# Kernel tuning notes

Hardware: AMD Instinct MI355X
Metric: run time of the kernel (lower is better)

The kernel has to match this reference:

```python
import jax, jax.numpy as jnp
import numpy as np

ALPHA = 0.1          # LeakyReLU negative slope
NEG = -9.0e15        # mask fill value (matches torch source)
S_OUT = 64           # source_out_features
T_OUT = 64           # target_out_features


def setup_inputs() -> dict:
    key = jax.random.key(0)
    ks = jax.random.split(key, 8)
    n_s, n_t = 8192, 4096
    s_in, t_in = 128, 128
    hs = jax.random.normal(ks[0], (n_s, s_in), dtype=jnp.float32)
    ht = jax.random.normal(ks[1], (n_t, t_in), dtype=jnp.float32)
    A_opt = jax.random.randint(ks[2], (n_t, n_s), 0, 2, dtype=jnp.int32)
    # xavier_uniform with gain=1.414
    def xavier(k, shape, gain=1.414):
        fan_in, fan_out = shape[0], shape[1]
        bound = gain * np.sqrt(6.0 / (fan_in + fan_out))
        return jax.random.uniform(k, shape, jnp.float32, -bound, bound)
    Ws = xavier(ks[3], (s_in, T_OUT))
    Wt = xavier(ks[4], (t_in, S_OUT))
    a1 = xavier(ks[5], (S_OUT + T_OUT, 1))
    bias_s = jnp.zeros((T_OUT,), jnp.float32)
    bias_t = jnp.zeros((S_OUT,), jnp.float32)
    return {"hs": hs, "ht": ht, "A_opt": A_opt, "Ws": Ws, "Wt": Wt,
            "a1": a1, "bias_s": bias_s, "bias_t": bias_t}


def reference(hs, ht, A_opt, Ws, Wt, a1, bias_s, bias_t):
    # Asymmetric HOAN, eval mode (dropout=0), concatenate=True.
    Whs = hs @ Ws                       # [n_s, t_out]
    Wht = ht @ Wt                       # [n_t, s_out]
    # a1 split: first S_OUT rows pair with Wht, remaining T_OUT rows with Whs
    a_t = a1[:S_OUT, :]                 # [s_out, 1]
    a_s = a1[S_OUT:, :]                 # [t_out, 1]
    Whst = Whs @ a_s                    # [n_s, 1]
    Whtt = Wht @ a_t                    # [n_t, 1]
    e_st = jax.nn.leaky_relu(Whtt + Whst.T, ALPHA)   # [n_t, n_s]
    e_ts = jax.nn.leaky_relu(Whst + Whtt.T, ALPHA)   # [n_s, n_t]
    mask = A_opt > 0                    # [n_t, n_s]
    att_st = jax.nn.softmax(jnp.where(mask, e_st, NEG), axis=1)
    h_prime_st = att_st @ Whs + bias_s  # [n_t, t_out]
    att_ts = jax.nn.softmax(jnp.where(mask.T, e_ts, NEG), axis=1)
    h_prime_ts = att_ts @ Wht + bias_t  # [n_s, s_out]
    return jax.nn.elu(h_prime_st), jax.nn.elu(h_prime_ts)
```

## Files before the change

### kernel.cpp

```cpp
#include <hip/hip_runtime.h>
#include <math.h>

#define N_S 8192
#define N_T 4096
#define DIN 128
#define NF  64
#define SPL0 8
#define SPL1 8

typedef __attribute__((ext_vector_type(8))) short short8;
typedef __attribute__((ext_vector_type(4))) float f32x4;
typedef unsigned long long u64;
typedef unsigned int u32;

__device__ __forceinline__ unsigned short f2bf(float x){
  unsigned u = __float_as_uint(x);
  unsigned r = (u + 0x7fffu + ((u >> 16) & 1u)) >> 16;
  return (unsigned short)r;
}

__device__ __forceinline__ size_t xt2_idx(int f, int k){
  return ((size_t)(k >> 5))*2048 + (size_t)((f >> 4)*512 + ((k >> 3) & 3)*128 + (f & 15)*8 + (k & 7));
}

__global__ __launch_bounds__(256) void k1_fused(
    const int* __restrict__ A,
    u64* __restrict__ RBt,
    u64* __restrict__ CBt,
    const float* __restrict__ hs, const float* __restrict__ ht,
    const float* __restrict__ Ws, const float* __restrict__ Wt,
    const float* __restrict__ a1,
    unsigned short* __restrict__ XT2s, unsigned short* __restrict__ XT2t,
    float* __restrict__ Es, float* __restrict__ Fs,
    float* __restrict__ Et, float* __restrict__ Ft)
{
  __shared__ __align__(16) float smem[DIN*NF + 4*DIN];
  int bx = blockIdx.x;
  int t = threadIdx.x;
  if (bx < 2048) {
    unsigned* T4 = (unsigned*)smem;
    int i0 = (bx & 63) * 64;
    int j0 = (bx >> 6) * 256;
    int w = t >> 6, l = t & 63;
    int4 v[16];
    #pragma unroll
    for (int it = 0; it < 16; ++it)
      v[it] = *(const int4*)&A[(size_t)(i0 + w*16 + it)*N_S + j0 + 4*l];
    #pragma unroll
    for (int rg = 0; rg < 4; ++rg) {
      unsigned p = 0;
      #pragma unroll
      for (int rr = 0; rr < 4; ++rr) {
        int4 m = v[rg*4 + rr];
        unsigned nib = (m.x > 0 ? 1u : 0u) | (m.y > 0 ? 2u : 0u)
                     | (m.z > 0 ? 4u : 0u) | (m.w > 0 ? 8u : 0u);
        p |= nib << (8*rr);
      }
      T4[(w*4 + rg)*65 + l] = p;
    }
    __syncthreads();
    {
      int r = t & 63, g = t >> 6;
      u64 bits = 0;
      #pragma unroll
      for (int i = 0; i < 16; ++i) {
        unsigned word = T4[(r >> 2)*65 + g*16 + i];
        unsigned nib = (word >> (8*(r & 3))) & 0xFu;
        bits |= (u64)nib << (4*i);
      }
      RBt[(size_t)((j0 >> 6) + g)*N_T + i0 + r] = bits;
    }
    {
      int c = t;
      u64 bits = 0;
      #pragma unroll
      for (int rg = 0; rg < 16; ++rg) {
        unsigned word = T4[rg*65 + (c >> 2)];
        unsigned x = (word >> (c & 3)) & 0x01010101u;
        unsigned nib = (x * 0x01020408u) >> 24;
        bits |= (u64)(nib & 0xFu) << (4*rg);
      }
      CBt[(size_t)(i0 >> 6)*N_S + j0 + c] = bits;
    }
  } else {
    int b = bx - 2048;
    float* Wl = smem;
    float* hrow = smem + DIN*NF;
    bool is_s = b < (N_S/4);
    const float* h; const float* W; const float* av;
    unsigned short* XT; float* Ed; float* Fd; int r0;
    if (is_s) { r0 = b*4;           h = hs; W = Ws; av = a1 + 64; XT = XT2s; Ed = Es; Fd = Fs; }
    else      { r0 = (b - N_S/4)*4; h = ht; W = Wt; av = a1;      XT = XT2t; Ed = Et; Fd = Ft; }
    for (int i = t; i < DIN*NF; i += 256) Wl[i] = W[i];
    for (int i = t; i < 4*DIN;  i += 256) hrow[i] = h[(size_t)r0*DIN + i];
    __syncthreads();
    int f = t & 63, sr = t >> 6;
    float acc = 0.f;
    #pragma unroll 8
    for (int k = 0; k < DIN; ++k) acc += hrow[sr*DIN + k] * Wl[k*NF + f];
    int r = r0 + sr;
    XT[xt2_idx(f, r)] = f2bf(acc);
    float p = acc * av[f];
    #pragma unroll
    for (int o = 32; o > 0; o >>= 1) p += __shfl_xor(p, o, 64);
    if (f == 0) { Ed[r] = __expf(p); Fd[r] = __expf(0.1f*p); }
  }
}

template<int DIR>
__device__ __forceinline__ void agg_body(
    int rb, int split,
    const u64* __restrict__ MBt,
    const float* __restrict__ EuT, const float* __restrict__ FuT,
    const float* __restrict__ EkT, const float* __restrict__ FkT,
    const unsigned short* __restrict__ XT2,
    float* __restrict__ accP,
    float* __restrict__ sumP)
{
  constexpr int NK = (DIR == 0) ? N_S : N_T;
  constexpr int NU = (DIR == 0) ? N_T : N_S;
  constexpr int SPL = (DIR == 0) ? SPL0 : SPL1;
  constexpr int KCH = NK / SPL;
  int t = threadIdx.x;
  int wave = t >> 6, l = t & 63;
  int row16 = l & 15, grp = l >> 4;
  int u = rb*64 + wave*16 + row16;
  float Eu = EuT[u], Fu = FuT[u];
  f32x4 acc[4];
  #pragma unroll
  for (int q = 0; q < 4; ++q) { acc[q][0]=0.f; acc[q][1]=0.f; acc[q][2]=0.f; acc[q][3]=0.f; }
  f32x4 accs; accs[0]=0.f; accs[1]=0.f; accs[2]=0.f; accs[3]=0.f;
  short8 bones;
  #pragma unroll
  for (int j = 0; j < 8; ++j) bones[j] = (short)0x3F80;
  int kc0 = split * KCH;

  #pragma unroll 2
  for (int k0 = kc0; k0 < kc0 + KCH; k0 += 64) {
    u64 mb = MBt[(size_t)(k0 >> 6)*NU + u];
    u32 mlo = (u32)mb, mhi = (u32)(mb >> 32);
    short8 af01[2];
    #pragma unroll
    for (int h = 0; h < 2; ++h) {
      int kb = k0 + 32*h + grp*8;
      float4 e0 = *(const float4*)&EkT[kb];
      float4 e1 = *(const float4*)&EkT[kb + 4];
      float4 f0 = *(const float4*)&FkT[kb];
      float4 f1 = *(const float4*)&FkT[kb + 4];
      float w0 = fmaxf(Eu*e0.x, Fu*f0.x);
      float w1 = fmaxf(Eu*e0.y, Fu*f0.y);
      float w2 = fmaxf(Eu*e0.z, Fu*f0.z);
      float w3 = fmaxf(Eu*e0.w, Fu*f0.w);
      float w4 = fmaxf(Eu*e1.x, Fu*f1.x);
      float w5 = fmaxf(Eu*e1.y, Fu*f1.y);
      float w6 = fmaxf(Eu*e1.z, Fu*f1.z);
      float w7 = fmaxf(Eu*e1.w, Fu*f1.w);
      u32 bb = ((h ? mhi : mlo) >> (grp*8)) & 0xffu;
      float wv[8] = {w0,w1,w2,w3,w4,w5,w6,w7};
      union { u32 uu[4]; short8 v; } pk;
      #pragma unroll
      for (int p = 0; p < 4; ++p) {
        int j = 2*p;
        int slo = ((int)(bb << (31 - j))) >> 31;
        int shi = ((int)(bb << (30 - j))) >> 31;
        u32 msk = __builtin_amdgcn_perm((u32)shi, (u32)slo, 0x05040100u);
        u32 w01 = __builtin_amdgcn_perm(__float_as_uint(wv[j+1]),
                                        __float_as_uint(wv[j]), 0x07060302u);
        pk.uu[p] = w01 & msk;
      }
      af01[h] = pk.v;
    }
    const unsigned short* xb = XT2 + ((size_t)(k0 >> 5))*2048 + l*8;
    #pragma unroll
    for (int q = 0; q < 4; ++q) {
      short8 b0 = *(const short8*)(xb + q*512);
      short8 b1 = *(const short8*)(xb + 2048 + q*512);
      acc[q] = __builtin_amdgcn_mfma_f32_16x16x32_bf16(af01[0], b0, acc[q], 0, 0, 0);
      acc[q] = __builtin_amdgcn_mfma_f32_16x16x32_bf16(af01[1], b1, acc[q], 0, 0, 0);
    }
    accs = __builtin_amdgcn_mfma_f32_16x16x32_bf16(af01[0], bones, accs, 0, 0, 0);
    accs = __builtin_amdgcn_mfma_f32_16x16x32_bf16(af01[1], bones, accs, 0, 0, 0);
  }

  if (row16 == 0) {
    #pragma unroll
    for (int r = 0; r < 4; ++r)
      sumP[(size_t)split*NU + rb*64 + wave*16 + grp*4 + r] = accs[r];
  }
  float* ap = accP + (size_t)split*NU*NF;
  #pragma unroll
  for (int q = 0; q < 4; ++q) {
    #pragma unroll
    for (int r = 0; r < 4; ++r) {
      int uo = rb*64 + wave*16 + grp*4 + r;
      ap[(size_t)uo*NF + q*16 + row16] = acc[q][r];
    }
  }
}

__global__ __launch_bounds__(256, 8) void agg_fused(
    const u64* __restrict__ RBt, const u64* __restrict__ CBt,
    const float* __restrict__ Es, const float* __restrict__ Fs,
    const float* __restrict__ Et, const float* __restrict__ Ft,
    const unsigned short* __restrict__ XT2s, const unsigned short* __restrict__ XT2t,
    float* __restrict__ P0, float* __restrict__ S0,
    float* __restrict__ P1, float* __restrict__ S1)
{
  int b = blockIdx.x;
  if (b < 64*SPL0) {
    agg_body<0>(b & 63, b >> 6, RBt, Et, Ft, Es, Fs, XT2s, P0, S0);
  } else {
    int b2 = b - 64*SPL0;
    agg_body<1>(b2 & 127, b2 >> 7, CBt, Es, Fs, Et, Ft, XT2t, P1, S1);
  }
}

__global__ __launch_bounds__(256) void finalize_kernel(
    const float* __restrict__ P0, const float* __restrict__ S0,
    const float* __restrict__ P1, const float* __restrict__ S1,
    const float* __restrict__ bias_s, const float* __restrict__ bias_t,
    float* __restrict__ out)
{
  int tid = blockIdx.x*256 + threadIdx.x;
  const int n0 = N_T*NF/4;
  float4 a = make_float4(0.f, 0.f, 0.f, 0.f);
  float den = 0.f;
  float4 bias;
  if (tid < n0) {
    int u = tid >> 4, fq = (tid & 15)*4;
    #pragma unroll
    for (int s = 0; s < SPL0; ++s) {
      float4 p = *(const float4*)&P0[((size_t)s*N_T + u)*NF + fq];
      a.x += p.x; a.y += p.y; a.z += p.z; a.w += p.w;
      den += S0[(size_t)s*N_T + u];
    }
    bias = *(const float4*)&bias_s[fq];
  } else {
    int i2 = tid - n0;
    int u = i2 >> 4, fq = (i2 & 15)*4;
    #pragma unroll
    for (int s = 0; s < SPL1; ++s) {
      float4 p = *(const float4*)&P1[((size_t)s*N_S + u)*NF + fq];
      a.x += p.x; a.y += p.y; a.z += p.z; a.w += p.w;
      den += S1[(size_t)s*N_S + u];
    }
    bias = *(const float4*)&bias_t[fq];
  }
  float inv = den > 0.f ? 1.f/den : 0.f;
  float4 v;
  v.x = a.x*inv + bias.x; v.y = a.y*inv + bias.y;
  v.z = a.z*inv + bias.z; v.w = a.w*inv + bias.w;
  v.x = v.x > 0.f ? v.x : expm1f(v.x);
  v.y = v.y > 0.f ? v.y : expm1f(v.y);
  v.z = v.z > 0.f ? v.z : expm1f(v.z);
  v.w = v.w > 0.f ? v.w : expm1f(v.w);
  *(float4*)&out[tid*4] = v;
}

extern "C" void kernel_launch(void* const* d_in, const int* in_sizes, int n_in,
                              void* d_out, int out_size, void* d_ws, size_t ws_size,
                              hipStream_t stream)
{
  const float* hs     = (const float*)d_in[0];
  const float* ht     = (const float*)d_in[1];
  const int*   A      = (const int*)  d_in[2];
  const float* Ws     = (const float*)d_in[3];
  const float* Wt     = (const float*)d_in[4];
  const float* a1     = (const float*)d_in[5];
  const float* bias_s = (const float*)d_in[6];
  const float* bias_t = (const float*)d_in[7];
  float* out = (float*)d_out;

  u64* RBt = (u64*)d_ws;
  u64* CBt = RBt + (size_t)(N_S/64)*N_T;
  unsigned short* XT2s = (unsigned short*)(CBt + (size_t)(N_T/64)*N_S);
  unsigned short* XT2t = XT2s + (size_t)NF*N_S;
  float* Es = (float*)(XT2t + (size_t)NF*N_T);
  float* Fs = Es + N_S;
  float* Et = Fs + N_S;
  float* Ft = Et + N_T;
  float* P0 = Ft + N_T;
  float* S0 = P0 + (size_t)SPL0*N_T*NF;
  float* P1 = S0 + (size_t)SPL0*N_T;
  float* S1 = P1 + (size_t)SPL1*N_S*NF;

  k1_fused<<<2048 + (N_S + N_T)/4, 256, 0, stream>>>(A, RBt, CBt, hs, ht, Ws, Wt, a1,
                                                     XT2s, XT2t, Es, Fs, Et, Ft);
  agg_fused<<<64*SPL0 + 128*SPL1, 256, 0, stream>>>(RBt, CBt, Es, Fs, Et, Ft,
                                                    XT2s, XT2t, P0, S0, P1, S1);
  finalize_kernel<<<(N_T*NF + N_S*NF)/1024, 256, 0, stream>>>(P0, S0, P1, S1,
                                                              bias_s, bias_t, out);
}
```

Before: 89.58 us.

## Fuse finalize into aggregation via last-block counters, interleave E/F, halve split

Removes the separate finalize kernel. Each row block now keeps an atomic counter, and whichever split block finishes last reduces the partial sums, applies bias and ELU, and writes the output. E and F factors are interleaved into one array so a single vector load fetches both, and the target-direction split count drops from 8 to 4, giving fewer partials but also fewer blocks for that direction. This saves one launch and the partial-buffer reread, at the cost of threadfences, an atomic per block, and a serial tail handled by the last block.

```diff
diff --git a/kernel.cpp b/kernel.cpp
--- a/kernel.cpp
+++ b/kernel.cpp
@@ -6,7 +6,7 @@
 #define DIN 128
 #define NF  64
 #define SPL0 8
-#define SPL1 8
+#define SPL1 4
 
 typedef __attribute__((ext_vector_type(8))) short short8;
 typedef __attribute__((ext_vector_type(4))) float f32x4;
@@ -31,12 +31,13 @@
     const float* __restrict__ Ws, const float* __restrict__ Wt,
     const float* __restrict__ a1,
     unsigned short* __restrict__ XT2s, unsigned short* __restrict__ XT2t,
-    float* __restrict__ Es, float* __restrict__ Fs,
-    float* __restrict__ Et, float* __restrict__ Ft)
+    float* __restrict__ EFs, float* __restrict__ EFt,
+    int* __restrict__ cnt)
 {
   __shared__ __align__(16) float smem[DIN*NF + 4*DIN];
   int bx = blockIdx.x;
   int t = threadIdx.x;
+  if (bx == 0 && t < 192) cnt[t] = 0;
   if (bx < 2048) {
     unsigned* T4 = (unsigned*)smem;
     int i0 = (bx & 63) * 64;
@@ -88,9 +89,9 @@
     float* hrow = smem + DIN*NF;
     bool is_s = b < (N_S/4);
     const float* h; const float* W; const float* av;
-    unsigned short* XT; float* Ed; float* Fd; int r0;
-    if (is_s) { r0 = b*4;           h = hs; W = Ws; av = a1 + 64; XT = XT2s; Ed = Es; Fd = Fs; }
-    else      { r0 = (b - N_S/4)*4; h = ht; W = Wt; av = a1;      XT = XT2t; Ed = Et; Fd = Ft; }
+    unsigned short* XT; float* EFd; int r0;
+    if (is_s) { r0 = b*4;           h = hs; W = Ws; av = a1 + 64; XT = XT2s; EFd = EFs; }
+    else      { r0 = (b - N_S/4)*4; h = ht; W = Wt; av = a1;      XT = XT2t; EFd = EFt; }
     for (int i = t; i < DIN*NF; i += 256) Wl[i] = W[i];
     for (int i = t; i < 4*DIN;  i += 256) hrow[i] = h[(size_t)r0*DIN + i];
     __syncthreads();
@@ -103,7 +104,7 @@
     float p = acc * av[f];
     #pragma unroll
     for (int o = 32; o > 0; o >>= 1) p += __shfl_xor(p, o, 64);
-    if (f == 0) { Ed[r] = __expf(p); Fd[r] = __expf(0.1f*p); }
+    if (f == 0) { EFd[2*r] = __expf(p); EFd[2*r + 1] = __expf(0.1f*p); }
   }
 }
 
@@ -111,11 +112,13 @@
 __device__ __forceinline__ void agg_body(
     int rb, int split,
     const u64* __restrict__ MBt,
-    const float* __restrict__ EuT, const float* __restrict__ FuT,
-    const float* __restrict__ EkT, const float* __restrict__ FkT,
+    const float* __restrict__ EFu, const float* __restrict__ EFk,
     const unsigned short* __restrict__ XT2,
     float* __restrict__ accP,
-    float* __restrict__ sumP)
+    float* __restrict__ sumP,
+    int* __restrict__ cnt,
+    const float* __restrict__ bias,
+    float* __restrict__ outB)
 {
   constexpr int NK = (DIR == 0) ? N_S : N_T;
   constexpr int NU = (DIR == 0) ? N_T : N_S;
@@ -125,7 +128,8 @@
   int wave = t >> 6, l = t & 63;
   int row16 = l & 15, grp = l >> 4;
   int u = rb*64 + wave*16 + row16;
-  float Eu = EuT[u], Fu = FuT[u];
+  float2 ef = *(const float2*)&EFu[2*u];
+  float Eu = ef.x, Fu = ef.y;
   f32x4 acc[4];
   #pragma unroll
   for (int q = 0; q < 4; ++q) { acc[q][0]=0.f; acc[q][1]=0.f; acc[q][2]=0.f; acc[q][3]=0.f; }
@@ -143,20 +147,16 @@
     #pragma unroll
     for (int h = 0; h < 2; ++h) {
       int kb = k0 + 32*h + grp*8;
-      float4 e0 = *(const float4*)&EkT[kb];
-      float4 e1 = *(const float4*)&EkT[kb + 4];
-      float4 f0 = *(const float4*)&FkT[kb];
-      float4 f1 = *(const float4*)&FkT[kb + 4];
-      float w0 = fmaxf(Eu*e0.x, Fu*f0.x);
-      float w1 = fmaxf(Eu*e0.y, Fu*f0.y);
-      float w2 = fmaxf(Eu*e0.z, Fu*f0.z);
-      float w3 = fmaxf(Eu*e0.w, Fu*f0.w);
-      float w4 = fmaxf(Eu*e1.x, Fu*f1.x);
-      float w5 = fmaxf(Eu*e1.y, Fu*f1.y);
-      float w6 = fmaxf(Eu*e1.z, Fu*f1.z);
-      float w7 = fmaxf(Eu*e1.w, Fu*f1.w);
+      float4 p0 = *(const float4*)&EFk[2*kb];
+      float4 p1 = *(const float4*)&EFk[2*kb + 4];
+      float4 p2 = *(const float4*)&EFk[2*kb + 8];
+      float4 p3 = *(const float4*)&EFk[2*kb + 12];
+      float wv[8];
+      wv[0] = fmaxf(Eu*p0.x, Fu*p0.y); wv[1] = fmaxf(Eu*p0.z, Fu*p0.w);
+      wv[2] = fmaxf(Eu*p1.x, Fu*p1.y); wv[3] = fmaxf(Eu*p1.z, Fu*p1.w);
+      wv[4] = fmaxf(Eu*p2.x, Fu*p2.y); wv[5] = fmaxf(Eu*p2.z, Fu*p2.w);
+      wv[6] = fmaxf(Eu*p3.x, Fu*p3.y); wv[7] = fmaxf(Eu*p3.z, Fu*p3.w);
       u32 bb = ((h ? mhi : mlo) >> (grp*8)) & 0xffu;
-      float wv[8] = {w0,w1,w2,w3,w4,w5,w6,w7};
       union { u32 uu[4]; short8 v; } pk;
       #pragma unroll
       for (int p = 0; p < 4; ++p) {
@@ -196,65 +196,60 @@
       ap[(size_t)uo*NF + q*16 + row16] = acc[q][r];
     }
   }
-}
-
-__global__ __launch_bounds__(256, 8) void agg_fused(
+
+  __shared__ int sflag;
+  __threadfence();
+  __syncthreads();
+  if (t == 0) sflag = (atomicAdd(cnt, 1) == SPL - 1);
+  __syncthreads();
+  if (!sflag) return;
+  __threadfence();
+  #pragma unroll
+  for (int q = 0; q < 4; ++q) {
+    int item = t + 256*q;
+    int row = item >> 4, f4 = item & 15;
+    int uu = rb*64 + row;
+    float4 a = make_float4(0.f, 0.f, 0.f, 0.f);
+    float den = 0.f;
+    #pragma unroll
+    for (int s = 0; s < SPL; ++s) {
+      float4 p = *(const float4*)&accP[((size_t)s*NU + uu)*NF + f4*4];
+      a.x += p.x; a.y += p.y; a.z += p.z; a.w += p.w;
+      den += sumP[(size_t)s*NU + uu];
+    }
+    float4 b4 = *(const float4*)&bias[f4*4];
+    float inv = den > 0.f ? 1.f/den : 0.f;
+    float4 v;
+    v.x = a.x*inv + b4.x; v.y = a.y*inv + b4.y;
+    v.z = a.z*inv + b4.z; v.w = a.w*inv + b4.w;
+    v.x = v.x > 0.f ? v.x : expm1f(v.x);
+    v.y = v.y > 0.f ? v.y : expm1f(v.y);
+    v.z = v.z > 0.f ? v.z : expm1f(v.z);
+    v.w = v.w > 0.f ? v.w : expm1f(v.w);
+    *(float4*)&outB[(size_t)uu*NF + f4*4] = v;
+  }
+}
+
+__global__ __launch_bounds__(256, 8) void agg_fin(
     const u64* __restrict__ RBt, const u64* __restrict__ CBt,
-    const float* __restrict__ Es, const float* __restrict__ Fs,
-    const float* __restrict__ Et, const float* __restrict__ Ft,
+    const float* __restrict__ EFs, const float* __restrict__ EFt,
     const unsigned short* __restrict__ XT2s, const unsigned short* __restrict__ XT2t,
     float* __restrict__ P0, float* __restrict__ S0,
-    float* __restrict__ P1, float* __restrict__ S1)
+    float* __restrict__ P1, float* __restrict__ S1,
+    int* __restrict__ cnt,
+    const float* __restrict__ bias_s, const float* __restrict__ bias_t,
+    float* __restrict__ out)
 {
   int b = blockIdx.x;
   if (b < 64*SPL0) {
-    agg_body<0>(b & 63, b >> 6, RBt, Et, Ft, Es, Fs, XT2s, P0, S0);
+    int rb = b & 63;
+    agg_body<0>(rb, b >> 6, RBt, EFt, EFs, XT2s, P0, S0, cnt + rb, bias_s, out);
   } else {
     int b2 = b - 64*SPL0;
-    agg_body<1>(b2 & 127, b2 >> 7, CBt, Es, Fs, Et, Ft, XT2t, P1, S1);
-  }
-}
-
-__global__ __launch_bounds__(256) void finalize_kernel(
-    const float* __restrict__ P0, const float* __restrict__ S0,
-    const float* __restrict__ P1, const float* __restrict__ S1,
-    const float* __restrict__ bias_s, const float* __restrict__ bias_t,
-    float* __restrict__ out)
-{
-  int tid = blockIdx.x*256 + threadIdx.x;
-  const int n0 = N_T*NF/4;
-  float4 a = make_float4(0.f, 0.f, 0.f, 0.f);
-  float den = 0.f;
-  float4 bias;
-  if (tid < n0) {
-    int u = tid >> 4, fq = (tid & 15)*4;
-    #pragma unroll
-    for (int s = 0; s < SPL0; ++s) {
-      float4 p = *(const float4*)&P0[((size_t)s*N_T + u)*NF + fq];
-      a.x += p.x; a.y += p.y; a.z += p.z; a.w += p.w;
-      den += S0[(size_t)s*N_T + u];
-    }
-    bias = *(const float4*)&bias_s[fq];
-  } else {
-    int i2 = tid - n0;
-    int u = i2 >> 4, fq = (i2 & 15)*4;
-    #pragma unroll
-    for (int s = 0; s < SPL1; ++s) {
-      float4 p = *(const float4*)&P1[((size_t)s*N_S + u)*NF + fq];
-      a.x += p.x; a.y += p.y; a.z += p.z; a.w += p.w;
-      den += S1[(size_t)s*N_S + u];
-    }
-    bias = *(const float4*)&bias_t[fq];
-  }
-  float inv = den > 0.f ? 1.f/den : 0.f;
-  float4 v;
-  v.x = a.x*inv + bias.x; v.y = a.y*inv + bias.y;
-  v.z = a.z*inv + bias.z; v.w = a.w*inv + bias.w;
-  v.x = v.x > 0.f ? v.x : expm1f(v.x);
-  v.y = v.y > 0.f ? v.y : expm1f(v.y);
-  v.z = v.z > 0.f ? v.z : expm1f(v.z);
-  v.w = v.w > 0.f ? v.w : expm1f(v.w);
-  *(float4*)&out[tid*4] = v;
+    int rb = b2 & 127;
+    agg_body<1>(rb, b2 >> 7, CBt, EFs, EFt, XT2t, P1, S1, cnt + 64 + rb, bias_t,
+                out + (size_t)N_T*NF);
+  }
 }
 
 extern "C" void kernel_launch(void* const* d_in, const int* in_sizes, int n_in,
@@ -275,19 +270,16 @@
   u64* CBt = RBt + (size_t)(N_S/64)*N_T;
   unsigned short* XT2s = (unsigned short*)(CBt + (size_t)(N_T/64)*N_S);
   unsigned short* XT2t = XT2s + (size_t)NF*N_S;
-  float* Es = (float*)(XT2t + (size_t)NF*N_T);
-  float* Fs = Es + N_S;
-  float* Et = Fs + N_S;
-  float* Ft = Et + N_T;
-  float* P0 = Ft + N_T;
-  float* S0 = P0 + (size_t)SPL0*N_T*NF;
-  float* P1 = S0 + (size_t)SPL0*N_T;
-  float* S1 = P1 + (size_t)SPL1*N_S*NF;
+  float* EFs = (float*)(XT2t + (size_t)NF*N_T);
+  float* EFt = EFs + 2*N_S;
+  float* P0  = EFt + 2*N_T;
+  float* S0  = P0 + (size_t)SPL0*N_T*NF;
+  float* P1  = S0 + (size_t)SPL0*N_T;
+  float* S1  = P1 + (size_t)SPL1*N_S*NF;
+  int*   cnt = (int*)(S1 + (size_t)SPL1*N_S);
 
   k1_fused<<<2048 + (N_S + N_T)/4, 256, 0, stream>>>(A, RBt, CBt, hs, ht, Ws, Wt, a1,
-                                                     XT2s, XT2t, Es, Fs, Et, Ft);
-  agg_fused<<<64*SPL0 + 128*SPL1, 256, 0, stream>>>(RBt, CBt, Es, Fs, Et, Ft,
-                                                    XT2s, XT2t, P0, S0, P1, S1);
-  finalize_kernel<<<(N_T*NF + N_S*NF)/1024, 256, 0, stream>>>(P0, S0, P1, S1,
-                                                              bias_s, bias_t, out);
-}
+                                                     XT2s, XT2t, EFs, EFt, cnt);
+  agg_fin<<<64*SPL0 + 128*SPL1, 256, 0, stream>>>(RBt, CBt, EFs, EFt, XT2s, XT2t,
+                                                  P0, S0, P1, S1, cnt, bias_s, bias_t, out);
+}
```

New measurement: 233.4 us. 161% more time.
